# Performance work log

Measured on AMD Instinct MI355X. Metric: run time of the kernel, lower is better.

Reference implementation:

```python
import jax, jax.numpy as jnp
import numpy as np

B, S, N, D = 8, 4096, 1024, 1024
NUM_WIDTH, WIDTH_DIM, MAX_WIDTH = 64, 64, 32


def setup_inputs() -> dict:
    key = jax.random.key(0)
    k_seq, k_start, k_width, k_w, k_emb = jax.random.split(key, 5)
    sequence_tensor = jax.random.normal(k_seq, (B, S, D), dtype=jnp.float32)
    starts = jax.random.randint(k_start, (B, N), 0, S)
    widths = jax.random.randint(k_width, (B, N), 0, MAX_WIDTH)
    ends = jnp.minimum(starts + widths, S - 1)
    span_indices = jnp.stack([starts, ends], axis=-1).astype(jnp.int64)
    att_weight = jax.random.normal(k_w, (1, D), dtype=jnp.float32) * 0.02
    att_bias = jnp.zeros((1,), dtype=jnp.float32)
    width_embedding = jax.random.normal(k_emb, (NUM_WIDTH, WIDTH_DIM), dtype=jnp.float32) * 0.02
    return {
        "sequence_tensor": sequence_tensor,
        "span_indices": span_indices,
        "att_weight": att_weight,
        "att_bias": att_bias,
        "width_embedding": width_embedding,
    }


def _span_attend(sequence_tensor, span_indices, att_weight, att_bias):
    # per-token attention logit: (B, S)
    logits = jnp.einsum("bsd,d->bs", sequence_tensor, att_weight[0]) + att_bias[0]
    starts = span_indices[..., 0]  # (B, N)
    ends = span_indices[..., 1]    # (B, N)
    valid = (starts >= 0) & (ends >= starts)  # (B, N)
    pos = jnp.arange(sequence_tensor.shape[1])  # (S,)
    # membership mask: (B, N, S)
    in_span = (pos[None, None, :] >= starts[..., None]) & (pos[None, None, :] <= ends[..., None])
    neg_inf = jnp.asarray(-jnp.inf, logits.dtype)
    scores = jnp.where(in_span, logits[:, None, :], neg_inf)  # (B, N, S)
    # stable masked softmax; fully-masked rows yield all-zero weights
    m = jnp.max(scores, axis=-1, keepdims=True)
    m = jnp.where(jnp.isfinite(m), m, 0.0)
    e = jnp.exp(scores - m)
    denom = jnp.sum(e, axis=-1, keepdims=True)
    attn = e / jnp.where(denom > 0, denom, 1.0)  # (B, N, S)
    span_emb = jnp.einsum("bns,bsd->bnd", attn, sequence_tensor)  # (B, N, D)
    span_emb = jnp.where(valid[..., None], span_emb, 0.0)
    return span_emb, starts, ends


def reference(sequence_tensor, span_indices, att_weight, att_bias, width_embedding):
    span_emb, starts, ends = _span_attend(sequence_tensor, span_indices, att_weight, att_bias)
    widths = jnp.clip(ends - starts, 0, NUM_WIDTH - 1)  # (B, N)
    width_emb = width_embedding[widths]  # (B, N, WIDTH_DIM)
    return jnp.concatenate([span_emb, width_emb], axis=-1)
```

## Files before the change

kernel.cpp:

```cpp
#include <hip/hip_runtime.h>

#define BB 8
#define SS 4096
#define NN 1024
#define DD 1024
#define NUM_WIDTH 64
#define WIDTH_DIM 64
#define OUTD (DD + WIDTH_DIM)
#define NSPAN (BB * NN)
#define NBUCK 128
#define NBINS (BB * NBUCK)

__global__ __launch_bounds__(1024) void sort_kernel(const int2* __restrict__ idx2,
                                                    int4* __restrict__ meta) {
    __shared__ int cnt[NBINS];
    __shared__ int wsum[16];
    int tid = threadIdx.x, lane = tid & 63, wid = tid >> 6;
    cnt[tid] = 0;
    __syncthreads();

    for (int i = tid; i < NSPAN; i += 1024) {
        int2 se = idx2[i];
        int s0 = se.x > 0 ? se.x : 0;
        if (s0 > SS - 1) s0 = SS - 1;
        atomicAdd(&cnt[(i >> 10) * NBUCK + (s0 >> 5)], 1);
    }
    __syncthreads();

    int orig = cnt[tid];
    int x = orig;
    #pragma unroll
    for (int d = 1; d < 64; d <<= 1) {
        int y = __shfl_up(x, d, 64);
        if (lane >= d) x += y;
    }
    if (lane == 63) wsum[wid] = x;
    __syncthreads();
    if (wid == 0) {
        int s = (lane < 16) ? wsum[lane] : 0;
        #pragma unroll
        for (int d = 1; d < 16; d <<= 1) {
            int y = __shfl_up(s, d, 64);
            if (lane >= d) s += y;
        }
        if (lane < 16) wsum[lane] = s;
    }
    __syncthreads();
    int excl = x - orig + (wid > 0 ? wsum[wid - 1] : 0);
    __syncthreads();
    cnt[tid] = excl;
    __syncthreads();

    for (int i = tid; i < NSPAN; i += 1024) {
        int2 se = idx2[i];
        int s0 = se.x > 0 ? se.x : 0;
        if (s0 > SS - 1) s0 = SS - 1;
        int pos = atomicAdd(&cnt[(i >> 10) * NBUCK + (s0 >> 5)], 1);
        meta[pos] = make_int4(i, se.x, se.y, 0);
    }
}

__global__ __launch_bounds__(256) void span_kernel(const float* __restrict__ seq,
                                                   const float* __restrict__ w,
                                                   const float* __restrict__ wemb,
                                                   const int4* __restrict__ meta,
                                                   float* __restrict__ out) {
    int swz = (blockIdx.x & 7) * (NSPAN / 8) + (blockIdx.x >> 3);
    int4 me = meta[swz];
    int bn = me.x, start = me.y, end = me.z;
    int b  = bn >> 10;
    int tid = threadIdx.x;
    int wave = tid >> 6;
    int lane = tid & 63;

    int s0 = start > 0 ? start : 0;
    int e0 = end < (SS - 1) ? end : (SS - 1);
    int L  = (start >= 0 && end >= start) ? (e0 - s0 + 1) : 0;
    if (L < 0) L = 0;
    if (L > 32) L = 32;

    if (tid < WIDTH_DIM) {
        int wdt = end - start;
        if (wdt < 0) wdt = 0;
        if (wdt > NUM_WIDTH - 1) wdt = NUM_WIDTH - 1;
        out[(long long)bn * OUTD + DD + tid] = wemb[wdt * WIDTH_DIM + tid];
    }

    __shared__ float lds_acc[4][DD];
    __shared__ float lds_m[4], lds_z[4];

    const float4* s4 = (const float4*)(seq + ((long long)b * SS + s0) * DD);
    const float4* w4 = (const float4*)w;
    float4 wr0 = w4[lane], wr1 = w4[64 + lane], wr2 = w4[128 + lane], wr3 = w4[192 + lane];

    float m = -INFINITY, Z = 0.f;
    float4 acc0 = make_float4(0.f, 0.f, 0.f, 0.f);
    float4 acc1 = acc0, acc2 = acc0, acc3 = acc0;

    int r = wave;
    for (; r + 4 < L; r += 8) {
        const float4* rowA = s4 + (long long)r * (DD / 4);
        const float4* rowB = rowA + DD;
        float4 a0 = rowA[lane], a1 = rowA[64 + lane], a2 = rowA[128 + lane], a3 = rowA[192 + lane];
        float4 b0 = rowB[lane], b1 = rowB[64 + lane], b2 = rowB[128 + lane], b3 = rowB[192 + lane];
        float dA = a0.x * wr0.x + a0.y * wr0.y + a0.z * wr0.z + a0.w * wr0.w
                 + a1.x * wr1.x + a1.y * wr1.y + a1.z * wr1.z + a1.w * wr1.w
                 + a2.x * wr2.x + a2.y * wr2.y + a2.z * wr2.z + a2.w * wr2.w
                 + a3.x * wr3.x + a3.y * wr3.y + a3.z * wr3.z + a3.w * wr3.w;
        float dB = b0.x * wr0.x + b0.y * wr0.y + b0.z * wr0.z + b0.w * wr0.w
                 + b1.x * wr1.x + b1.y * wr1.y + b1.z * wr1.z + b1.w * wr1.w
                 + b2.x * wr2.x + b2.y * wr2.y + b2.z * wr2.z + b2.w * wr2.w
                 + b3.x * wr3.x + b3.y * wr3.y + b3.z * wr3.z + b3.w * wr3.w;
        #pragma unroll
        for (int d = 32; d >= 1; d >>= 1) {
            dA += __shfl_xor(dA, d, 64);
            dB += __shfl_xor(dB, d, 64);
        }
        float dm = fmaxf(dA, dB);
        if (dm > m) {
            float f = __expf(m - dm);
            Z *= f;
            acc0.x *= f; acc0.y *= f; acc0.z *= f; acc0.w *= f;
            acc1.x *= f; acc1.y *= f; acc1.z *= f; acc1.w *= f;
            acc2.x *= f; acc2.y *= f; acc2.z *= f; acc2.w *= f;
            acc3.x *= f; acc3.y *= f; acc3.z *= f; acc3.w *= f;
            m = dm;
        }
        float eA = __expf(dA - m);
        float eB = __expf(dB - m);
        Z += eA + eB;
        acc0.x += eA * a0.x + eB * b0.x; acc0.y += eA * a0.y + eB * b0.y;
        acc0.z += eA * a0.z + eB * b0.z; acc0.w += eA * a0.w + eB * b0.w;
        acc1.x += eA * a1.x + eB * b1.x; acc1.y += eA * a1.y + eB * b1.y;
        acc1.z += eA * a1.z + eB * b1.z; acc1.w += eA * a1.w + eB * b1.w;
        acc2.x += eA * a2.x + eB * b2.x; acc2.y += eA * a2.y + eB * b2.y;
        acc2.z += eA * a2.z + eB * b2.z; acc2.w += eA * a2.w + eB * b2.w;
        acc3.x += eA * a3.x + eB * b3.x; acc3.y += eA * a3.y + eB * b3.y;
        acc3.z += eA * a3.z + eB * b3.z; acc3.w += eA * a3.w + eB * b3.w;
    }
    if (r < L) {
        const float4* rowA = s4 + (long long)r * (DD / 4);
        float4 a0 = rowA[lane], a1 = rowA[64 + lane], a2 = rowA[128 + lane], a3 = rowA[192 + lane];
        float dA = a0.x * wr0.x + a0.y * wr0.y + a0.z * wr0.z + a0.w * wr0.w
                 + a1.x * wr1.x + a1.y * wr1.y + a1.z * wr1.z + a1.w * wr1.w
                 + a2.x * wr2.x + a2.y * wr2.y + a2.z * wr2.z + a2.w * wr2.w
                 + a3.x * wr3.x + a3.y * wr3.y + a3.z * wr3.z + a3.w * wr3.w;
        #pragma unroll
        for (int d = 32; d >= 1; d >>= 1)
            dA += __shfl_xor(dA, d, 64);
        if (dA > m) {
            float f = __expf(m - dA);
            Z *= f;
            acc0.x *= f; acc0.y *= f; acc0.z *= f; acc0.w *= f;
            acc1.x *= f; acc1.y *= f; acc1.z *= f; acc1.w *= f;
            acc2.x *= f; acc2.y *= f; acc2.z *= f; acc2.w *= f;
            acc3.x *= f; acc3.y *= f; acc3.z *= f; acc3.w *= f;
            m = dA;
        }
        float eA = __expf(dA - m);
        Z += eA;
        acc0.x += eA * a0.x; acc0.y += eA * a0.y; acc0.z += eA * a0.z; acc0.w += eA * a0.w;
        acc1.x += eA * a1.x; acc1.y += eA * a1.y; acc1.z += eA * a1.z; acc1.w += eA * a1.w;
        acc2.x += eA * a2.x; acc2.y += eA * a2.y; acc2.z += eA * a2.z; acc2.w += eA * a2.w;
        acc3.x += eA * a3.x; acc3.y += eA * a3.y; acc3.z += eA * a3.z; acc3.w += eA * a3.w;
    }

    if (lane == 0) { lds_m[wave] = m; lds_z[wave] = Z; }
    float4* la = (float4*)lds_acc[wave];
    la[lane] = acc0; la[64 + lane] = acc1; la[128 + lane] = acc2; la[192 + lane] = acc3;
    __syncthreads();

    float m0 = lds_m[0], m1 = lds_m[1], m2 = lds_m[2], m3 = lds_m[3];
    float mg = fmaxf(fmaxf(m0, m1), fmaxf(m2, m3));
    float f0 = (m0 == -INFINITY) ? 0.f : __expf(m0 - mg);
    float f1 = (m1 == -INFINITY) ? 0.f : __expf(m1 - mg);
    float f2 = (m2 == -INFINITY) ? 0.f : __expf(m2 - mg);
    float f3 = (m3 == -INFINITY) ? 0.f : __expf(m3 - mg);
    float Zg = f0 * lds_z[0] + f1 * lds_z[1] + f2 * lds_z[2] + f3 * lds_z[3];
    float inv = (Zg > 0.f) ? 1.0f / Zg : 0.f;

    float4 r0 = ((float4*)lds_acc[0])[tid];
    float4 r1 = ((float4*)lds_acc[1])[tid];
    float4 r2 = ((float4*)lds_acc[2])[tid];
    float4 r3 = ((float4*)lds_acc[3])[tid];
    float4 o;
    o.x = (f0 * r0.x + f1 * r1.x + f2 * r2.x + f3 * r3.x) * inv;
    o.y = (f0 * r0.y + f1 * r1.y + f2 * r2.y + f3 * r3.y) * inv;
    o.z = (f0 * r0.z + f1 * r1.z + f2 * r2.z + f3 * r3.z) * inv;
    o.w = (f0 * r0.w + f1 * r1.w + f2 * r2.w + f3 * r3.w) * inv;

    float4* o4 = (float4*)(out + (long long)bn * OUTD);
    o4[tid] = o;
}

extern "C" void kernel_launch(void* const* d_in, const int* in_sizes, int n_in,
                              void* d_out, int out_size, void* d_ws, size_t ws_size,
                              hipStream_t stream) {
    const float* seq  = (const float*)d_in[0];
    const int*   idx  = (const int*)d_in[1];
    const float* w    = (const float*)d_in[2];
    const float* wemb = (const float*)d_in[4];
    float* out = (float*)d_out;

    int4* meta = (int4*)d_ws;

    sort_kernel<<<1, 1024, 0, stream>>>((const int2*)idx, meta);
    span_kernel<<<NSPAN, 256, 0, stream>>>(seq, w, wemb, meta, out);
}
```

Before: 49.29 us.

## Use 8 waves per span with all row loads issued upfront and global max

The span kernel now runs 512 threads (8 waves). Each wave loads up to four rows at once, clamping out-of-range rows to a valid address, so every load for a span is in flight together instead of inside a serial loop. Softmax uses one block-wide max exchanged through LDS, so the online rescaling is gone and the final reduction is a plain sum over 8 partial accumulators. This costs an extra barrier, double the LDS footprint, 64 live float4 registers per thread, and redundant loads of clamped rows for short spans.

```diff
diff --git a/kernel.cpp b/kernel.cpp
--- a/kernel.cpp
+++ b/kernel.cpp
@@ -60,11 +60,11 @@
     }
 }
 
-__global__ __launch_bounds__(256) void span_kernel(const float* __restrict__ seq,
-                                                   const float* __restrict__ w,
-                                                   const float* __restrict__ wemb,
-                                                   const int4* __restrict__ meta,
-                                                   float* __restrict__ out) {
+__global__ __launch_bounds__(512, 4) void span_kernel(const float* __restrict__ seq,
+                                                      const float* __restrict__ w,
+                                                      const float* __restrict__ wemb,
+                                                      const int4* __restrict__ meta,
+                                                      float* __restrict__ out) {
     int swz = (blockIdx.x & 7) * (NSPAN / 8) + (blockIdx.x >> 3);
     int4 me = meta[swz];
     int bn = me.x, start = me.y, end = me.z;
@@ -74,8 +74,8 @@
     int lane = tid & 63;
 
     int s0 = start > 0 ? start : 0;
-    int e0 = end < (SS - 1) ? end : (SS - 1);
-    int L  = (start >= 0 && end >= start) ? (e0 - s0 + 1) : 0;
+    int eC = end < (SS - 1) ? end : (SS - 1);
+    int L  = (start >= 0 && end >= start) ? (eC - s0 + 1) : 0;
     if (L < 0) L = 0;
     if (L > 32) L = 32;
 
@@ -86,111 +86,106 @@
         out[(long long)bn * OUTD + DD + tid] = wemb[wdt * WIDTH_DIM + tid];
     }
 
-    __shared__ float lds_acc[4][DD];
-    __shared__ float lds_m[4], lds_z[4];
+    __shared__ float lds_acc[8][DD];
+    __shared__ float lds_wm[8];
+    __shared__ float lds_wz[8];
 
     const float4* s4 = (const float4*)(seq + ((long long)b * SS + s0) * DD);
     const float4* w4 = (const float4*)w;
     float4 wr0 = w4[lane], wr1 = w4[64 + lane], wr2 = w4[128 + lane], wr3 = w4[192 + lane];
 
-    float m = -INFINITY, Z = 0.f;
-    float4 acc0 = make_float4(0.f, 0.f, 0.f, 0.f);
-    float4 acc1 = acc0, acc2 = acc0, acc3 = acc0;
-
-    int r = wave;
-    for (; r + 4 < L; r += 8) {
-        const float4* rowA = s4 + (long long)r * (DD / 4);
-        const float4* rowB = rowA + DD;
-        float4 a0 = rowA[lane], a1 = rowA[64 + lane], a2 = rowA[128 + lane], a3 = rowA[192 + lane];
-        float4 b0 = rowB[lane], b1 = rowB[64 + lane], b2 = rowB[128 + lane], b3 = rowB[192 + lane];
-        float dA = a0.x * wr0.x + a0.y * wr0.y + a0.z * wr0.z + a0.w * wr0.w
-                 + a1.x * wr1.x + a1.y * wr1.y + a1.z * wr1.z + a1.w * wr1.w
-                 + a2.x * wr2.x + a2.y * wr2.y + a2.z * wr2.z + a2.w * wr2.w
-                 + a3.x * wr3.x + a3.y * wr3.y + a3.z * wr3.z + a3.w * wr3.w;
-        float dB = b0.x * wr0.x + b0.y * wr0.y + b0.z * wr0.z + b0.w * wr0.w
-                 + b1.x * wr1.x + b1.y * wr1.y + b1.z * wr1.z + b1.w * wr1.w
-                 + b2.x * wr2.x + b2.y * wr2.y + b2.z * wr2.z + b2.w * wr2.w
-                 + b3.x * wr3.x + b3.y * wr3.y + b3.z * wr3.z + b3.w * wr3.w;
-        #pragma unroll
-        for (int d = 32; d >= 1; d >>= 1) {
-            dA += __shfl_xor(dA, d, 64);
-            dB += __shfl_xor(dB, d, 64);
-        }
-        float dm = fmaxf(dA, dB);
-        if (dm > m) {
-            float f = __expf(m - dm);
-            Z *= f;
-            acc0.x *= f; acc0.y *= f; acc0.z *= f; acc0.w *= f;
-            acc1.x *= f; acc1.y *= f; acc1.z *= f; acc1.w *= f;
-            acc2.x *= f; acc2.y *= f; acc2.z *= f; acc2.w *= f;
-            acc3.x *= f; acc3.y *= f; acc3.z *= f; acc3.w *= f;
-            m = dm;
-        }
-        float eA = __expf(dA - m);
-        float eB = __expf(dB - m);
-        Z += eA + eB;
-        acc0.x += eA * a0.x + eB * b0.x; acc0.y += eA * a0.y + eB * b0.y;
-        acc0.z += eA * a0.z + eB * b0.z; acc0.w += eA * a0.w + eB * b0.w;
-        acc1.x += eA * a1.x + eB * b1.x; acc1.y += eA * a1.y + eB * b1.y;
-        acc1.z += eA * a1.z + eB * b1.z; acc1.w += eA * a1.w + eB * b1.w;
-        acc2.x += eA * a2.x + eB * b2.x; acc2.y += eA * a2.y + eB * b2.y;
-        acc2.z += eA * a2.z + eB * b2.z; acc2.w += eA * a2.w + eB * b2.w;
-        acc3.x += eA * a3.x + eB * b3.x; acc3.y += eA * a3.y + eB * b3.y;
-        acc3.z += eA * a3.z + eB * b3.z; acc3.w += eA * a3.w + eB * b3.w;
-    }
-    if (r < L) {
-        const float4* rowA = s4 + (long long)r * (DD / 4);
-        float4 a0 = rowA[lane], a1 = rowA[64 + lane], a2 = rowA[128 + lane], a3 = rowA[192 + lane];
-        float dA = a0.x * wr0.x + a0.y * wr0.y + a0.z * wr0.z + a0.w * wr0.w
-                 + a1.x * wr1.x + a1.y * wr1.y + a1.z * wr1.z + a1.w * wr1.w
-                 + a2.x * wr2.x + a2.y * wr2.y + a2.z * wr2.z + a2.w * wr2.w
-                 + a3.x * wr3.x + a3.y * wr3.y + a3.z * wr3.z + a3.w * wr3.w;
-        #pragma unroll
-        for (int d = 32; d >= 1; d >>= 1)
-            dA += __shfl_xor(dA, d, 64);
-        if (dA > m) {
-            float f = __expf(m - dA);
-            Z *= f;
-            acc0.x *= f; acc0.y *= f; acc0.z *= f; acc0.w *= f;
-            acc1.x *= f; acc1.y *= f; acc1.z *= f; acc1.w *= f;
-            acc2.x *= f; acc2.y *= f; acc2.z *= f; acc2.w *= f;
-            acc3.x *= f; acc3.y *= f; acc3.z *= f; acc3.w *= f;
-            m = dA;
-        }
-        float eA = __expf(dA - m);
-        Z += eA;
-        acc0.x += eA * a0.x; acc0.y += eA * a0.y; acc0.z += eA * a0.z; acc0.w += eA * a0.w;
-        acc1.x += eA * a1.x; acc1.y += eA * a1.y; acc1.z += eA * a1.z; acc1.w += eA * a1.w;
-        acc2.x += eA * a2.x; acc2.y += eA * a2.y; acc2.z += eA * a2.z; acc2.w += eA * a2.w;
-        acc3.x += eA * a3.x; acc3.y += eA * a3.y; acc3.z += eA * a3.z; acc3.w += eA * a3.w;
-    }
-
-    if (lane == 0) { lds_m[wave] = m; lds_z[wave] = Z; }
+    int lm1 = (L > 0) ? (L - 1) : 0;
+    bool v0 = (wave      ) < L;  int rc0 = v0 ? (wave     ) : lm1;
+    bool v1 = (wave +  8 ) < L;  int rc1 = v1 ? (wave +  8) : lm1;
+    bool v2 = (wave + 16 ) < L;  int rc2 = v2 ? (wave + 16) : lm1;
+    bool v3 = (wave + 24 ) < L;  int rc3 = v3 ? (wave + 24) : lm1;
+
+    const float4* p0 = s4 + (long long)rc0 * (DD / 4);
+    const float4* p1 = s4 + (long long)rc1 * (DD / 4);
+    const float4* p2 = s4 + (long long)rc2 * (DD / 4);
+    const float4* p3 = s4 + (long long)rc3 * (DD / 4);
+
+    float4 a00 = p0[lane], a01 = p0[64 + lane], a02 = p0[128 + lane], a03 = p0[192 + lane];
+    float4 a10 = p1[lane], a11 = p1[64 + lane], a12 = p1[128 + lane], a13 = p1[192 + lane];
+    float4 a20 = p2[lane], a21 = p2[64 + lane], a22 = p2[128 + lane], a23 = p2[192 + lane];
+    float4 a30 = p3[lane], a31 = p3[64 + lane], a32 = p3[128 + lane], a33 = p3[192 + lane];
+
+    float d0 = a00.x * wr0.x + a00.y * wr0.y + a00.z * wr0.z + a00.w * wr0.w
+             + a01.x * wr1.x + a01.y * wr1.y + a01.z * wr1.z + a01.w * wr1.w
+             + a02.x * wr2.x + a02.y * wr2.y + a02.z * wr2.z + a02.w * wr2.w
+             + a03.x * wr3.x + a03.y * wr3.y + a03.z * wr3.z + a03.w * wr3.w;
+    float d1 = a10.x * wr0.x + a10.y * wr0.y + a10.z * wr0.z + a10.w * wr0.w
+             + a11.x * wr1.x + a11.y * wr1.y + a11.z * wr1.z + a11.w * wr1.w
+             + a12.x * wr2.x + a12.y * wr2.y + a12.z * wr2.z + a12.w * wr2.w
+             + a13.x * wr3.x + a13.y * wr3.y + a13.z * wr3.z + a13.w * wr3.w;
+    float d2 = a20.x * wr0.x + a20.y * wr0.y + a20.z * wr0.z + a20.w * wr0.w
+             + a21.x * wr1.x + a21.y * wr1.y + a21.z * wr1.z + a21.w * wr1.w
+             + a22.x * wr2.x + a22.y * wr2.y + a22.z * wr2.z + a22.w * wr2.w
+             + a23.x * wr3.x + a23.y * wr3.y + a23.z * wr3.z + a23.w * wr3.w;
+    float d3 = a30.x * wr0.x + a30.y * wr0.y + a30.z * wr0.z + a30.w * wr0.w
+             + a31.x * wr1.x + a31.y * wr1.y + a31.z * wr1.z + a31.w * wr1.w
+             + a32.x * wr2.x + a32.y * wr2.y + a32.z * wr2.z + a32.w * wr2.w
+             + a33.x * wr3.x + a33.y * wr3.y + a33.z * wr3.z + a33.w * wr3.w;
+
+    #pragma unroll
+    for (int s = 32; s >= 1; s >>= 1) {
+        d0 += __shfl_xor(d0, s, 64);
+        d1 += __shfl_xor(d1, s, 64);
+        d2 += __shfl_xor(d2, s, 64);
+        d3 += __shfl_xor(d3, s, 64);
+    }
+
+    float mw = -INFINITY;
+    if (v0) mw = fmaxf(mw, d0);
+    if (v1) mw = fmaxf(mw, d1);
+    if (v2) mw = fmaxf(mw, d2);
+    if (v3) mw = fmaxf(mw, d3);
+    if (lane == 0) lds_wm[wave] = mw;
+    __syncthreads();
+
+    float mg = fmaxf(fmaxf(fmaxf(lds_wm[0], lds_wm[1]), fmaxf(lds_wm[2], lds_wm[3])),
+                     fmaxf(fmaxf(lds_wm[4], lds_wm[5]), fmaxf(lds_wm[6], lds_wm[7])));
+
+    float x0 = v0 ? __expf(d0 - mg) : 0.f;
+    float x1 = v1 ? __expf(d1 - mg) : 0.f;
+    float x2 = v2 ? __expf(d2 - mg) : 0.f;
+    float x3 = v3 ? __expf(d3 - mg) : 0.f;
+    if (lane == 0) lds_wz[wave] = x0 + x1 + x2 + x3;
+
+    float4 acc0, acc1, acc2, acc3;
+    acc0.x = x0 * a00.x + x1 * a10.x + x2 * a20.x + x3 * a30.x;
+    acc0.y = x0 * a00.y + x1 * a10.y + x2 * a20.y + x3 * a30.y;
+    acc0.z = x0 * a00.z + x1 * a10.z + x2 * a20.z + x3 * a30.z;
+    acc0.w = x0 * a00.w + x1 * a10.w + x2 * a20.w + x3 * a30.w;
+    acc1.x = x0 * a01.x + x1 * a11.x + x2 * a21.x + x3 * a31.x;
+    acc1.y = x0 * a01.y + x1 * a11.y + x2 * a21.y + x3 * a31.y;
+    acc1.z = x0 * a01.z + x1 * a11.z + x2 * a21.z + x3 * a31.z;
+    acc1.w = x0 * a01.w + x1 * a11.w + x2 * a21.w + x3 * a31.w;
+    acc2.x = x0 * a02.x + x1 * a12.x + x2 * a22.x + x3 * a32.x;
+    acc2.y = x0 * a02.y + x1 * a12.y + x2 * a22.y + x3 * a32.y;
+    acc2.z = x0 * a02.z + x1 * a12.z + x2 * a22.z + x3 * a32.z;
+    acc2.w = x0 * a02.w + x1 * a12.w + x2 * a22.w + x3 * a32.w;
+    acc3.x = x0 * a03.x + x1 * a13.x + x2 * a23.x + x3 * a33.x;
+    acc3.y = x0 * a03.y + x1 * a13.y + x2 * a23.y + x3 * a33.y;
+    acc3.z = x0 * a03.z + x1 * a13.z + x2 * a23.z + x3 * a33.z;
+    acc3.w = x0 * a03.w + x1 * a13.w + x2 * a23.w + x3 * a33.w;
+
     float4* la = (float4*)lds_acc[wave];
     la[lane] = acc0; la[64 + lane] = acc1; la[128 + lane] = acc2; la[192 + lane] = acc3;
     __syncthreads();
 
-    float m0 = lds_m[0], m1 = lds_m[1], m2 = lds_m[2], m3 = lds_m[3];
-    float mg = fmaxf(fmaxf(m0, m1), fmaxf(m2, m3));
-    float f0 = (m0 == -INFINITY) ? 0.f : __expf(m0 - mg);
-    float f1 = (m1 == -INFINITY) ? 0.f : __expf(m1 - mg);
-    float f2 = (m2 == -INFINITY) ? 0.f : __expf(m2 - mg);
-    float f3 = (m3 == -INFINITY) ? 0.f : __expf(m3 - mg);
-    float Zg = f0 * lds_z[0] + f1 * lds_z[1] + f2 * lds_z[2] + f3 * lds_z[3];
+    float Zg = lds_wz[0] + lds_wz[1] + lds_wz[2] + lds_wz[3]
+             + lds_wz[4] + lds_wz[5] + lds_wz[6] + lds_wz[7];
     float inv = (Zg > 0.f) ? 1.0f / Zg : 0.f;
 
-    float4 r0 = ((float4*)lds_acc[0])[tid];
-    float4 r1 = ((float4*)lds_acc[1])[tid];
-    float4 r2 = ((float4*)lds_acc[2])[tid];
-    float4 r3 = ((float4*)lds_acc[3])[tid];
-    float4 o;
-    o.x = (f0 * r0.x + f1 * r1.x + f2 * r2.x + f3 * r3.x) * inv;
-    o.y = (f0 * r0.y + f1 * r1.y + f2 * r2.y + f3 * r3.y) * inv;
-    o.z = (f0 * r0.z + f1 * r1.z + f2 * r2.z + f3 * r3.z) * inv;
-    o.w = (f0 * r0.w + f1 * r1.w + f2 * r2.w + f3 * r3.w) * inv;
-
-    float4* o4 = (float4*)(out + (long long)bn * OUTD);
-    o4[tid] = o;
+    float sx = 0.f, sy = 0.f;
+    #pragma unroll
+    for (int wv = 0; wv < 8; ++wv) {
+        float2 v = *(const float2*)&lds_acc[wv][2 * tid];
+        sx += v.x; sy += v.y;
+    }
+    float2 o = make_float2(sx * inv, sy * inv);
+    *(float2*)&out[(long long)bn * OUTD + 2 * tid] = o;
 }
 
 extern "C" void kernel_launch(void* const* d_in, const int* in_sizes, int n_in,
@@ -205,5 +200,5 @@
     int4* meta = (int4*)d_ws;
 
     sort_kernel<<<1, 1024, 0, stream>>>((const int2*)idx, meta);
-    span_kernel<<<NSPAN, 256, 0, stream>>>(seq, w, wemb, meta, out);
+    span_kernel<<<NSPAN, 512, 0, stream>>>(seq, w, wemb, meta, out);
 }
```

New measurement: 69.32 us. 1.41x slower.
